# Kernel optimization log

Hardware: AMD Instinct MI355X
Metric: run time of the kernel (lower is better)

The kernel has to match this reference:

```python
import jax, jax.numpy as jnp
import numpy as np

N_NODES = 100000
N_EDGES = 1600000
D_FEAT = 64


def setup_inputs() -> dict:
    key = jax.random.key(0)
    k1, k2 = jax.random.split(key)
    x = jax.random.normal(k1, (N_NODES, D_FEAT), dtype=jnp.float32)
    edge_index = jax.random.randint(k2, (2, N_EDGES), 0, N_NODES, dtype=jnp.int64)
    return {"x": x, "edge_index": edge_index}


def reference(x, edge_index):
    # LightGCN propagation: out = D^{-1/2} A D^{-1/2} x with A given in COO form.
    row, col = edge_index[0], edge_index[1]
    n = x.shape[0]
    # deg[i] = number of edges with row == i (torch.sparse.sum over dim=1 of ones)
    deg = jax.ops.segment_sum(jnp.ones_like(row, dtype=x.dtype), row, num_segments=n)
    deg_inv_sqrt = jnp.where(deg > 0, jax.lax.rsqrt(jnp.maximum(deg, 1.0)), 0.0)
    norm = deg_inv_sqrt[row] * deg_inv_sqrt[col]  # [E]
    # SpMM: out[row] += norm * x[col]  (gather-scale-scatter-reduce)
    messages = norm[:, None] * x[col]  # [E, d]
    out = jax.ops.segment_sum(messages, row, num_segments=n)  # [N, d]
    return out
```

## Files before the change

### kernel.cpp

```cpp
#include <hip/hip_runtime.h>
#include <hip/hip_fp16.h>

#define N_NODES 100000
#define D_FEAT 64
#define RPB 256
#define NB ((N_NODES + RPB - 1) / RPB)
#define CAP 6144
#define NCH 391
#define COL_BITS 17
#define COL_MASK ((1 << COL_BITS) - 1)

typedef float vfloat4 __attribute__((ext_vector_type(4)));

__global__ void __launch_bounds__(256)
count_kernel(const int* __restrict__ row, int* __restrict__ cnt, int E) {
    __shared__ int h[NB];
    int t = threadIdx.x, c = blockIdx.x;
    for (int i = t; i < NB; i += 256) h[i] = 0;
    __syncthreads();
    int ce = (E + NCH - 1) / NCH;
    int lo = c * ce;
    int hi = min(lo + ce, E);
    for (int e = lo + t; e < hi; e += 256)
        atomicAdd(&h[row[e] >> 8], 1);
    __syncthreads();
    for (int i = t; i < NB; i += 256)
        cnt[c * NB + i] = h[i];
}

__global__ void __launch_bounds__(512)
colscan_kernel(int* __restrict__ cnt, int* __restrict__ bucketCnt) {
    __shared__ int s[512];
    int b = blockIdx.x, t = threadIdx.x;
    int v = (t < NCH) ? cnt[t * NB + b] : 0;
    s[t] = v;
    __syncthreads();
    for (int o = 1; o < 512; o <<= 1) {
        int u = (t >= o) ? s[t - o] : 0;
        __syncthreads();
        s[t] += u;
        __syncthreads();
    }
    if (t < NCH) cnt[t * NB + b] = s[t] - v;
    if (t == NCH - 1) bucketCnt[b] = s[t];
}

__global__ void __launch_bounds__(256)
part_kernel(const int* __restrict__ row, const int* __restrict__ col,
            const int* __restrict__ cnt,
            int* __restrict__ packed, int E) {
    __shared__ int h[NB];
    __shared__ int rbase[NB];
    int t = threadIdx.x, c = blockIdx.x;
    for (int i = t; i < NB; i += 256) {
        h[i] = 0;
        rbase[i] = cnt[c * NB + i];
    }
    __syncthreads();
    int ce = (E + NCH - 1) / NCH;
    int lo = c * ce;
    int hi = min(lo + ce, E);
    for (int e = lo + t; e < hi; e += 256) {
        int r = row[e], cc = col[e];
        int bk = r >> 8;
        int pos = rbase[bk] + atomicAdd(&h[bk], 1);
        if (pos < CAP)
            packed[bk * CAP + pos] = ((r & (RPB - 1)) << COL_BITS) | cc;
    }
}

__global__ void __launch_bounds__(512)
csr_build_kernel(int* __restrict__ packed,
                 const int* __restrict__ bucketCnt,
                 int4* __restrict__ rowSED,
                 const float* __restrict__ x, __half* __restrict__ xs, int N) {
    __shared__ int ebuf[CAP];
    __shared__ int sbuf[CAP];
    __shared__ int cnt[RPB];
    __shared__ int scn[RPB];
    __shared__ int cur[RPB];
    __shared__ float disS[RPB];
    int b = blockIdx.x, t = threadIdx.x;
    int base = b * CAP;
    int n = min(bucketCnt[b], CAP);
    for (int i = t; i < n; i += 512) ebuf[i] = packed[base + i];
    if (t < RPB) cnt[t] = 0;
    __syncthreads();
    for (int i = t; i < n; i += 512)
        atomicAdd(&cnt[ebuf[i] >> COL_BITS], 1);
    __syncthreads();
    int v = 0;
    if (t < RPB) { v = cnt[t]; scn[t] = v; }
    __syncthreads();
    for (int o = 1; o < RPB; o <<= 1) {
        int u = 0;
        if (t < RPB && t >= o) u = scn[t - o];
        __syncthreads();
        if (t < RPB) scn[t] += u;
        __syncthreads();
    }
    if (t < RPB) {
        int ex = scn[t] - v;
        cur[t] = ex;
        float d = (v > 0) ? rsqrtf((float)v) : 0.0f;
        disS[t] = d;
        int r = b * RPB + t;
        if (r < N)
            rowSED[r] = make_int4(base + ex, base + ex + v, __float_as_int(d), 0);
    }
    __syncthreads();
    for (int i = t; i < n; i += 512) {
        int p = ebuf[i];
        int lr = p >> COL_BITS;
        int pos = atomicAdd(&cur[lr], 1);
        sbuf[pos] = p & COL_MASK;
    }
    __syncthreads();
    for (int i = t; i < n; i += 512)
        packed[base + i] = sbuf[i];
    long long rowBase = (long long)b * RPB;
    for (int i = t; i < RPB * (D_FEAT / 4); i += 512) {
        int lr = i >> 4;
        long long rr = rowBase + lr;
        if (rr < N) {
            const vfloat4* xp = (const vfloat4*)(x + (rr << 6) + ((i & 15) << 2));
            vfloat4 vv = __builtin_nontemporal_load(xp);
            float dd = disS[lr];
            __half2 h0 = __floats2half2_rn(dd * vv.x, dd * vv.y);
            __half2 h1 = __floats2half2_rn(dd * vv.z, dd * vv.w);
            uint2 u;
            u.x = *(unsigned int*)&h0;
            u.y = *(unsigned int*)&h1;
            *(uint2*)(xs + (rr << 6) + ((i & 15) << 2)) = u;
        }
    }
}

__device__ __forceinline__ void fmap(__half2* a, uint4 v, __half2 w2) {
    __half2* hp = (__half2*)&v;
    a[0] = __hfma2(hp[0], w2, a[0]);
    a[1] = __hfma2(hp[1], w2, a[1]);
    a[2] = __hfma2(hp[2], w2, a[2]);
    a[3] = __hfma2(hp[3], w2, a[3]);
}
__device__ __forceinline__ void addp(__half2* a, uint4 v) {
    __half2* hp = (__half2*)&v;
    a[0] = __hadd2(a[0], hp[0]);
    a[1] = __hadd2(a[1], hp[1]);
    a[2] = __hadd2(a[2], hp[2]);
    a[3] = __hadd2(a[3], hp[3]);
}

__device__ __forceinline__ void row_slow(const __half* __restrict__ xs,
                                         const int* __restrict__ csr_col,
                                         int s, int e, int g, int q, __half2* acc) {
    int j = s;
    for (; j + 32 <= e; j += 32) {
        int c0 = csr_col[j + g];
        int c1 = csr_col[j + 8 + g];
        int c2 = csr_col[j + 16 + g];
        int c3 = csr_col[j + 24 + g];
        uint4 v0 = *(const uint4*)(xs + (c0 << 6) + (q << 3));
        uint4 v1 = *(const uint4*)(xs + (c1 << 6) + (q << 3));
        uint4 v2 = *(const uint4*)(xs + (c2 << 6) + (q << 3));
        uint4 v3 = *(const uint4*)(xs + (c3 << 6) + (q << 3));
        addp(acc, v0); addp(acc, v1); addp(acc, v2); addp(acc, v3);
    }
    int last = e - 1;
    int n0 = j + g, n1 = n0 + 8, n2 = n0 + 16, n3 = n0 + 24;
    int i0 = max(min(n0, last), 0);
    int i1 = max(min(n1, last), 0);
    int i2 = max(min(n2, last), 0);
    int i3 = max(min(n3, last), 0);
    int c0 = csr_col[i0] & COL_MASK;
    int c1 = csr_col[i1] & COL_MASK;
    int c2 = csr_col[i2] & COL_MASK;
    int c3 = csr_col[i3] & COL_MASK;
    uint4 v0 = *(const uint4*)(xs + (c0 << 6) + (q << 3));
    uint4 v1 = *(const uint4*)(xs + (c1 << 6) + (q << 3));
    uint4 v2 = *(const uint4*)(xs + (c2 << 6) + (q << 3));
    uint4 v3 = *(const uint4*)(xs + (c3 << 6) + (q << 3));
    __half2 w0 = __float2half2_rn((n0 < e) ? 1.0f : 0.0f);
    __half2 w1 = __float2half2_rn((n1 < e) ? 1.0f : 0.0f);
    __half2 w2 = __float2half2_rn((n2 < e) ? 1.0f : 0.0f);
    __half2 w3 = __float2half2_rn((n3 < e) ? 1.0f : 0.0f);
    fmap(acc, v0, w0); fmap(acc, v1, w1); fmap(acc, v2, w2); fmap(acc, v3, w3);
}

__global__ void __launch_bounds__(512)
spmm_h8x2_kernel(const __half* __restrict__ xs,
                 const int4* __restrict__ rowSED,
                 const int* __restrict__ csr_col,
                 float* __restrict__ out, int N) {
    int wv = (int)((blockIdx.x * (long long)blockDim.x + threadIdx.x) >> 6);
    int r0 = wv * 2;
    if (r0 >= N) return;
    int r1 = r0 + 1;
    bool has1 = (r1 < N);
    int lane = threadIdx.x & 63;
    int g = lane >> 3;
    int q = lane & 7;
    int4 sed0 = rowSED[r0];
    int4 sed1 = has1 ? rowSED[r1] : make_int4(0, 0, 0, 0);
    int s0 = sed0.x, e0 = sed0.y;
    int s1 = sed1.x, e1 = sed1.y;
    __half2 z = __float2half2_rn(0.f);
    __half2 a0[4] = {z, z, z, z};
    __half2 a1[4] = {z, z, z, z};

    if (max(e0 - s0, e1 - s1) <= 32) {
        int l0 = e0 - 1, l1 = e1 - 1;
        int m00 = s0 + g, m01 = m00 + 8, m02 = m00 + 16, m03 = m00 + 24;
        int m10 = s1 + g, m11 = m10 + 8, m12 = m10 + 16, m13 = m10 + 24;
        int i00 = max(min(m00, l0), 0), i01 = max(min(m01, l0), 0);
        int i02 = max(min(m02, l0), 0), i03 = max(min(m03, l0), 0);
        int i10 = max(min(m10, l1), 0), i11 = max(min(m11, l1), 0);
        int i12 = max(min(m12, l1), 0), i13 = max(min(m13, l1), 0);
        int c00 = csr_col[i00] & COL_MASK, c01 = csr_col[i01] & COL_MASK;
        int c02 = csr_col[i02] & COL_MASK, c03 = csr_col[i03] & COL_MASK;
        int c10 = csr_col[i10] & COL_MASK, c11 = csr_col[i11] & COL_MASK;
        int c12 = csr_col[i12] & COL_MASK, c13 = csr_col[i13] & COL_MASK;
        uint4 v00 = *(const uint4*)(xs + (c00 << 6) + (q << 3));
        uint4 v01 = *(const uint4*)(xs + (c01 << 6) + (q << 3));
        uint4 v02 = *(const uint4*)(xs + (c02 << 6) + (q << 3));
        uint4 v03 = *(const uint4*)(xs + (c03 << 6) + (q << 3));
        uint4 v10 = *(const uint4*)(xs + (c10 << 6) + (q << 3));
        uint4 v11 = *(const uint4*)(xs + (c11 << 6) + (q << 3));
        uint4 v12 = *(const uint4*)(xs + (c12 << 6) + (q << 3));
        uint4 v13 = *(const uint4*)(xs + (c13 << 6) + (q << 3));
        __half2 w00 = __float2half2_rn((m00 < e0) ? 1.0f : 0.0f);
        __half2 w01 = __float2half2_rn((m01 < e0) ? 1.0f : 0.0f);
        __half2 w02 = __float2half2_rn((m02 < e0) ? 1.0f : 0.0f);
        __half2 w03 = __float2half2_rn((m03 < e0) ? 1.0f : 0.0f);
        __half2 w10 = __float2half2_rn((m10 < e1) ? 1.0f : 0.0f);
        __half2 w11 = __float2half2_rn((m11 < e1) ? 1.0f : 0.0f);
        __half2 w12 = __float2half2_rn((m12 < e1) ? 1.0f : 0.0f);
        __half2 w13 = __float2half2_rn((m13 < e1) ? 1.0f : 0.0f);
        fmap(a0, v00, w00); fmap(a0, v01, w01); fmap(a0, v02, w02); fmap(a0, v03, w03);
        fmap(a1, v10, w10); fmap(a1, v11, w11); fmap(a1, v12, w12); fmap(a1, v13, w13);
    } else {
        row_slow(xs, csr_col, s0, e0, g, q, a0);
        if (has1) row_slow(xs, csr_col, s1, e1, g, q, a1);
    }

    #pragma unroll
    for (int k = 0; k < 4; ++k) {
        int a = *(int*)&a0[k];
        int b8 = __shfl_xor(a, 8);  a0[k] = __hadd2(a0[k], *(__half2*)&b8);
        a = *(int*)&a0[k];
        int b16 = __shfl_xor(a, 16); a0[k] = __hadd2(a0[k], *(__half2*)&b16);
        a = *(int*)&a0[k];
        int b32 = __shfl_xor(a, 32); a0[k] = __hadd2(a0[k], *(__half2*)&b32);
        a = *(int*)&a1[k];
        int d8 = __shfl_xor(a, 8);  a1[k] = __hadd2(a1[k], *(__half2*)&d8);
        a = *(int*)&a1[k];
        int d16 = __shfl_xor(a, 16); a1[k] = __hadd2(a1[k], *(__half2*)&d16);
        a = *(int*)&a1[k];
        int d32 = __shfl_xor(a, 32); a1[k] = __hadd2(a1[k], *(__half2*)&d32);
    }
    if (g == 0) {
        float dr = __int_as_float(sed0.z);
        float2 f0 = __half22float2(a0[0]);
        float2 f1 = __half22float2(a0[1]);
        float2 f2 = __half22float2(a0[2]);
        float2 f3 = __half22float2(a0[3]);
        vfloat4 o0, o1;
        o0.x = dr * f0.x; o0.y = dr * f0.y; o0.z = dr * f1.x; o0.w = dr * f1.y;
        o1.x = dr * f2.x; o1.y = dr * f2.y; o1.z = dr * f3.x; o1.w = dr * f3.y;
        float* op = out + ((long long)r0 << 6) + (q << 3);
        __builtin_nontemporal_store(o0, (vfloat4*)op);
        __builtin_nontemporal_store(o1, (vfloat4*)(op + 4));
    } else if (g == 1 && has1) {
        float dr = __int_as_float(sed1.z);
        float2 f0 = __half22float2(a1[0]);
        float2 f1 = __half22float2(a1[1]);
        float2 f2 = __half22float2(a1[2]);
        float2 f3 = __half22float2(a1[3]);
        vfloat4 o0, o1;
        o0.x = dr * f0.x; o0.y = dr * f0.y; o0.z = dr * f1.x; o0.w = dr * f1.y;
        o1.x = dr * f2.x; o1.y = dr * f2.y; o1.z = dr * f3.x; o1.w = dr * f3.y;
        float* op = out + ((long long)r1 << 6) + (q << 3);
        __builtin_nontemporal_store(o0, (vfloat4*)op);
        __builtin_nontemporal_store(o1, (vfloat4*)(op + 4));
    }
}

__global__ void fb_deg_kernel(const int* __restrict__ row, float* __restrict__ deg, int E) {
    int i = blockIdx.x * blockDim.x + threadIdx.x;
    int stride = gridDim.x * blockDim.x;
    for (; i < E; i += stride) atomicAdd(&deg[row[i]], 1.0f);
}
__global__ void fb_dis_kernel(float* __restrict__ deg, int N) {
    int i = blockIdx.x * blockDim.x + threadIdx.x;
    if (i < N) { float d = deg[i]; deg[i] = (d > 0.0f) ? rsqrtf(d) : 0.0f; }
}
__global__ void fb_scatter_kernel(const float* __restrict__ x, const int* __restrict__ row,
                                  const int* __restrict__ col, const float* __restrict__ dis,
                                  float* __restrict__ out, long long total) {
    long long i = (long long)blockIdx.x * blockDim.x + threadIdx.x;
    long long stride = (long long)gridDim.x * blockDim.x;
    for (; i < total; i += stride) {
        int e = (int)(i >> 6);
        int d = (int)(i & 63);
        int r = row[e];
        int c = col[e];
        atomicAdd(&out[(long long)r * D_FEAT + d], dis[r] * dis[c] * x[(long long)c * D_FEAT + d]);
    }
}

extern "C" void kernel_launch(void* const* d_in, const int* in_sizes, int n_in,
                              void* d_out, int out_size, void* d_ws, size_t ws_size,
                              hipStream_t stream) {
    const float* x  = (const float*)d_in[0];
    const int*   ei = (const int*)d_in[1];
    int E = in_sizes[1] / 2;
    const int* row = ei;
    const int* col = ei + E;
    float* out = (float*)d_out;
    const int N = N_NODES;

    size_t need = (size_t)NB * CAP * 4 + (size_t)N * D_FEAT * 2
                + (size_t)N * 16 + (size_t)NCH * NB * 4 + (size_t)NB * 4;

    if (ws_size >= need) {
        char* ws = (char*)d_ws;
        int*    packed    = (int*)ws;    ws += (size_t)NB * CAP * 4;
        __half* xs        = (__half*)ws; ws += (size_t)N * D_FEAT * 2;
        int4*   rowSED    = (int4*)ws;   ws += (size_t)N * 16;
        int*    cnt       = (int*)ws;    ws += (size_t)NCH * NB * 4;
        int*    bucketCnt = (int*)ws;

        count_kernel<<<NCH, 256, 0, stream>>>(row, cnt, E);
        colscan_kernel<<<NB, 512, 0, stream>>>(cnt, bucketCnt);
        part_kernel<<<NCH, 256, 0, stream>>>(row, col, cnt, packed, E);
        csr_build_kernel<<<NB, 512, 0, stream>>>(packed, bucketCnt, rowSED, x, xs, N);
        int waves = (N + 1) / 2;
        spmm_h8x2_kernel<<<(waves + 7) / 8, 512, 0, stream>>>(xs, rowSED, packed, out, N);
        return;
    }

    float* deg = (float*)d_ws;
    (void)hipMemsetAsync(out, 0, (size_t)out_size * sizeof(float), stream);
    (void)hipMemsetAsync(deg, 0, (size_t)N * sizeof(float), stream);
    fb_deg_kernel<<<2048, 256, 0, stream>>>(row, deg, E);
    fb_dis_kernel<<<(N + 255) / 256, 256, 0, stream>>>(deg, N);
    fb_scatter_kernel<<<4096, 256, 0, stream>>>(x, row, col, deg, out, (long long)E * D_FEAT);
}
```

Measured before the change: 78.53 us.

## Fuse per-bucket CSR sort into SpMM kernel using shared-memory column lists

Moves the per-bucket counting sort out of the build kernel and into the SpMM kernel, which now keeps each bucket's sorted column indices in LDS and processes its 256 rows directly. The build kernel becomes a light degree and x-scaling pass, and the rowSED array plus the write-back of sorted packed data to global memory are removed. The SpMM kernel now runs only NB (391) blocks of 512 threads with about 50KB of LDS each, which lowers occupancy and parallelism compared with one wave per two rows across the whole grid. Degree counting is also done twice.

```diff
diff --git a/kernel.cpp b/kernel.cpp
--- a/kernel.cpp
+++ b/kernel.cpp
@@ -70,54 +70,23 @@
 }
 
 __global__ void __launch_bounds__(512)
-csr_build_kernel(int* __restrict__ packed,
-                 const int* __restrict__ bucketCnt,
-                 int4* __restrict__ rowSED,
-                 const float* __restrict__ x, __half* __restrict__ xs, int N) {
-    __shared__ int ebuf[CAP];
-    __shared__ int sbuf[CAP];
+rowdis_conv_kernel(const int* __restrict__ packed, const int* __restrict__ bucketCnt,
+                   const float* __restrict__ x, __half* __restrict__ xs, int N) {
     __shared__ int cnt[RPB];
-    __shared__ int scn[RPB];
-    __shared__ int cur[RPB];
     __shared__ float disS[RPB];
     int b = blockIdx.x, t = threadIdx.x;
     int base = b * CAP;
     int n = min(bucketCnt[b], CAP);
-    for (int i = t; i < n; i += 512) ebuf[i] = packed[base + i];
     if (t < RPB) cnt[t] = 0;
     __syncthreads();
     for (int i = t; i < n; i += 512)
-        atomicAdd(&cnt[ebuf[i] >> COL_BITS], 1);
-    __syncthreads();
-    int v = 0;
-    if (t < RPB) { v = cnt[t]; scn[t] = v; }
-    __syncthreads();
-    for (int o = 1; o < RPB; o <<= 1) {
-        int u = 0;
-        if (t < RPB && t >= o) u = scn[t - o];
-        __syncthreads();
-        if (t < RPB) scn[t] += u;
-        __syncthreads();
-    }
+        atomicAdd(&cnt[packed[base + i] >> COL_BITS], 1);
+    __syncthreads();
     if (t < RPB) {
-        int ex = scn[t] - v;
-        cur[t] = ex;
-        float d = (v > 0) ? rsqrtf((float)v) : 0.0f;
-        disS[t] = d;
-        int r = b * RPB + t;
-        if (r < N)
-            rowSED[r] = make_int4(base + ex, base + ex + v, __float_as_int(d), 0);
-    }
-    __syncthreads();
-    for (int i = t; i < n; i += 512) {
-        int p = ebuf[i];
-        int lr = p >> COL_BITS;
-        int pos = atomicAdd(&cur[lr], 1);
-        sbuf[pos] = p & COL_MASK;
-    }
-    __syncthreads();
-    for (int i = t; i < n; i += 512)
-        packed[base + i] = sbuf[i];
+        int v = cnt[t];
+        disS[t] = (v > 0) ? rsqrtf((float)v) : 0.0f;
+    }
+    __syncthreads();
     long long rowBase = (long long)b * RPB;
     for (int i = t; i < RPB * (D_FEAT / 4); i += 512) {
         int lr = i >> 4;
@@ -143,145 +112,133 @@
     a[2] = __hfma2(hp[2], w2, a[2]);
     a[3] = __hfma2(hp[3], w2, a[3]);
 }
-__device__ __forceinline__ void addp(__half2* a, uint4 v) {
-    __half2* hp = (__half2*)&v;
-    a[0] = __hadd2(a[0], hp[0]);
-    a[1] = __hadd2(a[1], hp[1]);
-    a[2] = __hadd2(a[2], hp[2]);
-    a[3] = __hadd2(a[3], hp[3]);
-}
-
-__device__ __forceinline__ void row_slow(const __half* __restrict__ xs,
-                                         const int* __restrict__ csr_col,
-                                         int s, int e, int g, int q, __half2* acc) {
-    int j = s;
-    for (; j + 32 <= e; j += 32) {
-        int c0 = csr_col[j + g];
-        int c1 = csr_col[j + 8 + g];
-        int c2 = csr_col[j + 16 + g];
-        int c3 = csr_col[j + 24 + g];
-        uint4 v0 = *(const uint4*)(xs + (c0 << 6) + (q << 3));
-        uint4 v1 = *(const uint4*)(xs + (c1 << 6) + (q << 3));
-        uint4 v2 = *(const uint4*)(xs + (c2 << 6) + (q << 3));
-        uint4 v3 = *(const uint4*)(xs + (c3 << 6) + (q << 3));
-        addp(acc, v0); addp(acc, v1); addp(acc, v2); addp(acc, v3);
-    }
-    int last = e - 1;
-    int n0 = j + g, n1 = n0 + 8, n2 = n0 + 16, n3 = n0 + 24;
-    int i0 = max(min(n0, last), 0);
-    int i1 = max(min(n1, last), 0);
-    int i2 = max(min(n2, last), 0);
-    int i3 = max(min(n3, last), 0);
-    int c0 = csr_col[i0] & COL_MASK;
-    int c1 = csr_col[i1] & COL_MASK;
-    int c2 = csr_col[i2] & COL_MASK;
-    int c3 = csr_col[i3] & COL_MASK;
-    uint4 v0 = *(const uint4*)(xs + (c0 << 6) + (q << 3));
-    uint4 v1 = *(const uint4*)(xs + (c1 << 6) + (q << 3));
-    uint4 v2 = *(const uint4*)(xs + (c2 << 6) + (q << 3));
-    uint4 v3 = *(const uint4*)(xs + (c3 << 6) + (q << 3));
-    __half2 w0 = __float2half2_rn((n0 < e) ? 1.0f : 0.0f);
-    __half2 w1 = __float2half2_rn((n1 < e) ? 1.0f : 0.0f);
-    __half2 w2 = __float2half2_rn((n2 < e) ? 1.0f : 0.0f);
-    __half2 w3 = __float2half2_rn((n3 < e) ? 1.0f : 0.0f);
-    fmap(acc, v0, w0); fmap(acc, v1, w1); fmap(acc, v2, w2); fmap(acc, v3, w3);
-}
 
 __global__ void __launch_bounds__(512)
-spmm_h8x2_kernel(const __half* __restrict__ xs,
-                 const int4* __restrict__ rowSED,
-                 const int* __restrict__ csr_col,
-                 float* __restrict__ out, int N) {
-    int wv = (int)((blockIdx.x * (long long)blockDim.x + threadIdx.x) >> 6);
-    int r0 = wv * 2;
-    if (r0 >= N) return;
-    int r1 = r0 + 1;
-    bool has1 = (r1 < N);
-    int lane = threadIdx.x & 63;
+csr_spmm_kernel(int* __restrict__ packed,
+                const int* __restrict__ bucketCnt,
+                const __half* __restrict__ xs,
+                float* __restrict__ out, int N) {
+    __shared__ int ebuf[CAP];
+    __shared__ int sbuf[CAP];
+    __shared__ int rs[RPB];
+    __shared__ int rv[RPB];
+    __shared__ int cur[RPB];
+    __shared__ int scn[RPB];
+    __shared__ float disS[RPB];
+    int b = blockIdx.x, t = threadIdx.x;
+    int base = b * CAP;
+    int n = min(bucketCnt[b], CAP);
+    for (int i = t; i < n; i += 512) ebuf[i] = packed[base + i];
+    if (t < RPB) { rs[t] = 0; rv[t] = 0; cur[t] = 0; scn[t] = 0; }
+    __syncthreads();
+    for (int i = t; i < n; i += 512)
+        atomicAdd(&rv[ebuf[i] >> COL_BITS], 1);
+    __syncthreads();
+    int v = 0;
+    if (t < RPB) { v = rv[t]; scn[t] = v; }
+    __syncthreads();
+    for (int o = 1; o < RPB; o <<= 1) {
+        int u = 0;
+        if (t < RPB && t >= o) u = scn[t - o];
+        __syncthreads();
+        if (t < RPB) scn[t] += u;
+        __syncthreads();
+    }
+    if (t < RPB) {
+        int ex = scn[t] - v;
+        rs[t] = ex;
+        cur[t] = ex;
+        disS[t] = (v > 0) ? rsqrtf((float)v) : 0.0f;
+    }
+    __syncthreads();
+    for (int i = t; i < n; i += 512) {
+        int p = ebuf[i];
+        int lr = p >> COL_BITS;
+        int pos = atomicAdd(&cur[lr], 1);
+        sbuf[pos] = p & COL_MASK;
+    }
+    __syncthreads();
+
+    int wv = t >> 6;
+    int lane = t & 63;
     int g = lane >> 3;
     int q = lane & 7;
-    int4 sed0 = rowSED[r0];
-    int4 sed1 = has1 ? rowSED[r1] : make_int4(0, 0, 0, 0);
-    int s0 = sed0.x, e0 = sed0.y;
-    int s1 = sed1.x, e1 = sed1.y;
+    long long rowBase = (long long)b * RPB;
     __half2 z = __float2half2_rn(0.f);
-    __half2 a0[4] = {z, z, z, z};
-    __half2 a1[4] = {z, z, z, z};
-
-    if (max(e0 - s0, e1 - s1) <= 32) {
-        int l0 = e0 - 1, l1 = e1 - 1;
-        int m00 = s0 + g, m01 = m00 + 8, m02 = m00 + 16, m03 = m00 + 24;
-        int m10 = s1 + g, m11 = m10 + 8, m12 = m10 + 16, m13 = m10 + 24;
-        int i00 = max(min(m00, l0), 0), i01 = max(min(m01, l0), 0);
-        int i02 = max(min(m02, l0), 0), i03 = max(min(m03, l0), 0);
-        int i10 = max(min(m10, l1), 0), i11 = max(min(m11, l1), 0);
-        int i12 = max(min(m12, l1), 0), i13 = max(min(m13, l1), 0);
-        int c00 = csr_col[i00] & COL_MASK, c01 = csr_col[i01] & COL_MASK;
-        int c02 = csr_col[i02] & COL_MASK, c03 = csr_col[i03] & COL_MASK;
-        int c10 = csr_col[i10] & COL_MASK, c11 = csr_col[i11] & COL_MASK;
-        int c12 = csr_col[i12] & COL_MASK, c13 = csr_col[i13] & COL_MASK;
-        uint4 v00 = *(const uint4*)(xs + (c00 << 6) + (q << 3));
-        uint4 v01 = *(const uint4*)(xs + (c01 << 6) + (q << 3));
-        uint4 v02 = *(const uint4*)(xs + (c02 << 6) + (q << 3));
-        uint4 v03 = *(const uint4*)(xs + (c03 << 6) + (q << 3));
-        uint4 v10 = *(const uint4*)(xs + (c10 << 6) + (q << 3));
-        uint4 v11 = *(const uint4*)(xs + (c11 << 6) + (q << 3));
-        uint4 v12 = *(const uint4*)(xs + (c12 << 6) + (q << 3));
-        uint4 v13 = *(const uint4*)(xs + (c13 << 6) + (q << 3));
-        __half2 w00 = __float2half2_rn((m00 < e0) ? 1.0f : 0.0f);
-        __half2 w01 = __float2half2_rn((m01 < e0) ? 1.0f : 0.0f);
-        __half2 w02 = __float2half2_rn((m02 < e0) ? 1.0f : 0.0f);
-        __half2 w03 = __float2half2_rn((m03 < e0) ? 1.0f : 0.0f);
-        __half2 w10 = __float2half2_rn((m10 < e1) ? 1.0f : 0.0f);
-        __half2 w11 = __float2half2_rn((m11 < e1) ? 1.0f : 0.0f);
-        __half2 w12 = __float2half2_rn((m12 < e1) ? 1.0f : 0.0f);
-        __half2 w13 = __float2half2_rn((m13 < e1) ? 1.0f : 0.0f);
-        fmap(a0, v00, w00); fmap(a0, v01, w01); fmap(a0, v02, w02); fmap(a0, v03, w03);
-        fmap(a1, v10, w10); fmap(a1, v11, w11); fmap(a1, v12, w12); fmap(a1, v13, w13);
-    } else {
-        row_slow(xs, csr_col, s0, e0, g, q, a0);
-        if (has1) row_slow(xs, csr_col, s1, e1, g, q, a1);
-    }
-
-    #pragma unroll
-    for (int k = 0; k < 4; ++k) {
-        int a = *(int*)&a0[k];
-        int b8 = __shfl_xor(a, 8);  a0[k] = __hadd2(a0[k], *(__half2*)&b8);
-        a = *(int*)&a0[k];
-        int b16 = __shfl_xor(a, 16); a0[k] = __hadd2(a0[k], *(__half2*)&b16);
-        a = *(int*)&a0[k];
-        int b32 = __shfl_xor(a, 32); a0[k] = __hadd2(a0[k], *(__half2*)&b32);
-        a = *(int*)&a1[k];
-        int d8 = __shfl_xor(a, 8);  a1[k] = __hadd2(a1[k], *(__half2*)&d8);
-        a = *(int*)&a1[k];
-        int d16 = __shfl_xor(a, 16); a1[k] = __hadd2(a1[k], *(__half2*)&d16);
-        a = *(int*)&a1[k];
-        int d32 = __shfl_xor(a, 32); a1[k] = __hadd2(a1[k], *(__half2*)&d32);
-    }
-    if (g == 0) {
-        float dr = __int_as_float(sed0.z);
-        float2 f0 = __half22float2(a0[0]);
-        float2 f1 = __half22float2(a0[1]);
-        float2 f2 = __half22float2(a0[2]);
-        float2 f3 = __half22float2(a0[3]);
-        vfloat4 o0, o1;
-        o0.x = dr * f0.x; o0.y = dr * f0.y; o0.z = dr * f1.x; o0.w = dr * f1.y;
-        o1.x = dr * f2.x; o1.y = dr * f2.y; o1.z = dr * f3.x; o1.w = dr * f3.y;
-        float* op = out + ((long long)r0 << 6) + (q << 3);
-        __builtin_nontemporal_store(o0, (vfloat4*)op);
-        __builtin_nontemporal_store(o1, (vfloat4*)(op + 4));
-    } else if (g == 1 && has1) {
-        float dr = __int_as_float(sed1.z);
-        float2 f0 = __half22float2(a1[0]);
-        float2 f1 = __half22float2(a1[1]);
-        float2 f2 = __half22float2(a1[2]);
-        float2 f3 = __half22float2(a1[3]);
-        vfloat4 o0, o1;
-        o0.x = dr * f0.x; o0.y = dr * f0.y; o0.z = dr * f1.x; o0.w = dr * f1.y;
-        o1.x = dr * f2.x; o1.y = dr * f2.y; o1.z = dr * f3.x; o1.w = dr * f3.y;
-        float* op = out + ((long long)r1 << 6) + (q << 3);
-        __builtin_nontemporal_store(o0, (vfloat4*)op);
-        __builtin_nontemporal_store(o1, (vfloat4*)(op + 4));
+    #pragma unroll 1
+    for (int p = 0; p < 16; ++p) {
+        int lr0 = wv * 32 + 2 * p;
+        int lr1 = lr0 + 1;
+        int s0 = rs[lr0], v0 = rv[lr0];
+        int s1 = rs[lr1], v1 = rv[lr1];
+        __half2 a0[4] = {z, z, z, z};
+        __half2 a1[4] = {z, z, z, z};
+        int mx = max(v0, v1);
+        for (int j = 0; j < mx; j += 32) {
+            int c0[4], c1[4];
+            __half2 w0[4], w1[4];
+            #pragma unroll
+            for (int k = 0; k < 4; ++k) {
+                int n0 = j + g + 8 * k;
+                int i0 = s0 + max(min(n0, v0 - 1), 0);
+                c0[k] = sbuf[min(i0, CAP - 1)];
+                w0[k] = __float2half2_rn((n0 < v0) ? 1.0f : 0.0f);
+                int i1 = s1 + max(min(n0, v1 - 1), 0);
+                c1[k] = sbuf[min(i1, CAP - 1)];
+                w1[k] = __float2half2_rn((n0 < v1) ? 1.0f : 0.0f);
+            }
+            uint4 g0[4], g1[4];
+            #pragma unroll
+            for (int k = 0; k < 4; ++k)
+                g0[k] = *(const uint4*)(xs + (c0[k] << 6) + (q << 3));
+            #pragma unroll
+            for (int k = 0; k < 4; ++k)
+                g1[k] = *(const uint4*)(xs + (c1[k] << 6) + (q << 3));
+            #pragma unroll
+            for (int k = 0; k < 4; ++k) { fmap(a0, g0[k], w0[k]); fmap(a1, g1[k], w1[k]); }
+        }
+        #pragma unroll
+        for (int k = 0; k < 4; ++k) {
+            int a = *(int*)&a0[k];
+            int b8 = __shfl_xor(a, 8);   a0[k] = __hadd2(a0[k], *(__half2*)&b8);
+            a = *(int*)&a0[k];
+            int b16 = __shfl_xor(a, 16); a0[k] = __hadd2(a0[k], *(__half2*)&b16);
+            a = *(int*)&a0[k];
+            int b32 = __shfl_xor(a, 32); a0[k] = __hadd2(a0[k], *(__half2*)&b32);
+            a = *(int*)&a1[k];
+            int d8 = __shfl_xor(a, 8);   a1[k] = __hadd2(a1[k], *(__half2*)&d8);
+            a = *(int*)&a1[k];
+            int d16 = __shfl_xor(a, 16); a1[k] = __hadd2(a1[k], *(__half2*)&d16);
+            a = *(int*)&a1[k];
+            int d32 = __shfl_xor(a, 32); a1[k] = __hadd2(a1[k], *(__half2*)&d32);
+        }
+        long long r0 = rowBase + lr0;
+        long long r1 = rowBase + lr1;
+        if (g == 0 && r0 < N) {
+            float dr = disS[lr0];
+            float2 f0 = __half22float2(a0[0]);
+            float2 f1 = __half22float2(a0[1]);
+            float2 f2 = __half22float2(a0[2]);
+            float2 f3 = __half22float2(a0[3]);
+            vfloat4 o0, o1;
+            o0.x = dr * f0.x; o0.y = dr * f0.y; o0.z = dr * f1.x; o0.w = dr * f1.y;
+            o1.x = dr * f2.x; o1.y = dr * f2.y; o1.z = dr * f3.x; o1.w = dr * f3.y;
+            float* op = out + (r0 << 6) + (q << 3);
+            __builtin_nontemporal_store(o0, (vfloat4*)op);
+            __builtin_nontemporal_store(o1, (vfloat4*)(op + 4));
+        } else if (g == 1 && r1 < N) {
+            float dr = disS[lr1];
+            float2 f0 = __half22float2(a1[0]);
+            float2 f1 = __half22float2(a1[1]);
+            float2 f2 = __half22float2(a1[2]);
+            float2 f3 = __half22float2(a1[3]);
+            vfloat4 o0, o1;
+            o0.x = dr * f0.x; o0.y = dr * f0.y; o0.z = dr * f1.x; o0.w = dr * f1.y;
+            o1.x = dr * f2.x; o1.y = dr * f2.y; o1.z = dr * f3.x; o1.w = dr * f3.y;
+            float* op = out + (r1 << 6) + (q << 3);
+            __builtin_nontemporal_store(o0, (vfloat4*)op);
+            __builtin_nontemporal_store(o1, (vfloat4*)(op + 4));
+        }
     }
 }
 
@@ -320,22 +277,20 @@
     const int N = N_NODES;
 
     size_t need = (size_t)NB * CAP * 4 + (size_t)N * D_FEAT * 2
-                + (size_t)N * 16 + (size_t)NCH * NB * 4 + (size_t)NB * 4;
+                + (size_t)NCH * NB * 4 + (size_t)NB * 4;
 
     if (ws_size >= need) {
         char* ws = (char*)d_ws;
         int*    packed    = (int*)ws;    ws += (size_t)NB * CAP * 4;
         __half* xs        = (__half*)ws; ws += (size_t)N * D_FEAT * 2;
-        int4*   rowSED    = (int4*)ws;   ws += (size_t)N * 16;
         int*    cnt       = (int*)ws;    ws += (size_t)NCH * NB * 4;
         int*    bucketCnt = (int*)ws;
 
         count_kernel<<<NCH, 256, 0, stream>>>(row, cnt, E);
         colscan_kernel<<<NB, 512, 0, stream>>>(cnt, bucketCnt);
         part_kernel<<<NCH, 256, 0, stream>>>(row, col, cnt, packed, E);
-        csr_build_kernel<<<NB, 512, 0, stream>>>(packed, bucketCnt, rowSED, x, xs, N);
-        int waves = (N + 1) / 2;
-        spmm_h8x2_kernel<<<(waves + 7) / 8, 512, 0, stream>>>(xs, rowSED, packed, out, N);
+        rowdis_conv_kernel<<<NB, 512, 0, stream>>>(packed, bucketCnt, x, xs, N);
+        csr_spmm_kernel<<<NB, 512, 0, stream>>>(packed, bucketCnt, xs, out, N);
         return;
     }
 
```

Result: slower. 82.39 us (+4.9%).

## Replace count+scan bucketing with per-chunk global atomic cursor reservation

Applied to the files above, without the earlier changes.

Removes the separate count and column-scan kernels. Each partition block now builds a local histogram of its edge chunk and reserves space in each bucket with one global atomicAdd per non-empty bucket, then scatters. This saves a full pass over row plus a scan kernel and a launch, at the cost of global atomics and a nondeterministic edge order within buckets. The order change can alter floating-point summation order.

```diff
diff --git a/kernel.cpp b/kernel.cpp
--- a/kernel.cpp
+++ b/kernel.cpp
@@ -6,72 +6,49 @@
 #define RPB 256
 #define NB ((N_NODES + RPB - 1) / RPB)
 #define CAP 6144
-#define NCH 391
+#define CHUNK 4096
 #define COL_BITS 17
 #define COL_MASK ((1 << COL_BITS) - 1)
 
 typedef float vfloat4 __attribute__((ext_vector_type(4)));
 
-__global__ void __launch_bounds__(256)
-count_kernel(const int* __restrict__ row, int* __restrict__ cnt, int E) {
-    __shared__ int h[NB];
-    int t = threadIdx.x, c = blockIdx.x;
-    for (int i = t; i < NB; i += 256) h[i] = 0;
-    __syncthreads();
-    int ce = (E + NCH - 1) / NCH;
-    int lo = c * ce;
-    int hi = min(lo + ce, E);
-    for (int e = lo + t; e < hi; e += 256)
-        atomicAdd(&h[row[e] >> 8], 1);
-    __syncthreads();
-    for (int i = t; i < NB; i += 256)
-        cnt[c * NB + i] = h[i];
-}
-
-__global__ void __launch_bounds__(512)
-colscan_kernel(int* __restrict__ cnt, int* __restrict__ bucketCnt) {
-    __shared__ int s[512];
-    int b = blockIdx.x, t = threadIdx.x;
-    int v = (t < NCH) ? cnt[t * NB + b] : 0;
-    s[t] = v;
-    __syncthreads();
-    for (int o = 1; o < 512; o <<= 1) {
-        int u = (t >= o) ? s[t - o] : 0;
-        __syncthreads();
-        s[t] += u;
-        __syncthreads();
-    }
-    if (t < NCH) cnt[t * NB + b] = s[t] - v;
-    if (t == NCH - 1) bucketCnt[b] = s[t];
+__global__ void zero_kernel(int* __restrict__ p, int n) {
+    int i = blockIdx.x * blockDim.x + threadIdx.x;
+    if (i < n) p[i] = 0;
 }
 
 __global__ void __launch_bounds__(256)
 part_kernel(const int* __restrict__ row, const int* __restrict__ col,
-            const int* __restrict__ cnt,
+            int* __restrict__ bucketCursor,
             int* __restrict__ packed, int E) {
     __shared__ int h[NB];
     __shared__ int rbase[NB];
-    int t = threadIdx.x, c = blockIdx.x;
+    int t = threadIdx.x;
+    for (int i = t; i < NB; i += 256) h[i] = 0;
+    __syncthreads();
+    int lo = blockIdx.x * CHUNK;
+    int hi = min(lo + CHUNK, E);
+    for (int e = lo + t; e < hi; e += 256)
+        atomicAdd(&h[row[e] >> 8], 1);
+    __syncthreads();
     for (int i = t; i < NB; i += 256) {
+        int c2 = h[i];
+        rbase[i] = c2 ? atomicAdd(&bucketCursor[i], c2) : 0;
         h[i] = 0;
-        rbase[i] = cnt[c * NB + i];
-    }
-    __syncthreads();
-    int ce = (E + NCH - 1) / NCH;
-    int lo = c * ce;
-    int hi = min(lo + ce, E);
+    }
+    __syncthreads();
     for (int e = lo + t; e < hi; e += 256) {
-        int r = row[e], cc = col[e];
+        int r = row[e], c = col[e];
         int bk = r >> 8;
         int pos = rbase[bk] + atomicAdd(&h[bk], 1);
         if (pos < CAP)
-            packed[bk * CAP + pos] = ((r & (RPB - 1)) << COL_BITS) | cc;
+            packed[bk * CAP + pos] = ((r & (RPB - 1)) << COL_BITS) | c;
     }
 }
 
 __global__ void __launch_bounds__(512)
 csr_build_kernel(int* __restrict__ packed,
-                 const int* __restrict__ bucketCnt,
+                 const int* __restrict__ bucketCursor,
                  int4* __restrict__ rowSED,
                  const float* __restrict__ x, __half* __restrict__ xs, int N) {
     __shared__ int ebuf[CAP];
@@ -82,7 +59,7 @@
     __shared__ float disS[RPB];
     int b = blockIdx.x, t = threadIdx.x;
     int base = b * CAP;
-    int n = min(bucketCnt[b], CAP);
+    int n = min(bucketCursor[b], CAP);
     for (int i = t; i < n; i += 512) ebuf[i] = packed[base + i];
     if (t < RPB) cnt[t] = 0;
     __syncthreads();
@@ -320,20 +297,19 @@
     const int N = N_NODES;
 
     size_t need = (size_t)NB * CAP * 4 + (size_t)N * D_FEAT * 2
-                + (size_t)N * 16 + (size_t)NCH * NB * 4 + (size_t)NB * 4;
+                + (size_t)N * 16 + (size_t)NB * 4;
 
     if (ws_size >= need) {
         char* ws = (char*)d_ws;
-        int*    packed    = (int*)ws;    ws += (size_t)NB * CAP * 4;
-        __half* xs        = (__half*)ws; ws += (size_t)N * D_FEAT * 2;
-        int4*   rowSED    = (int4*)ws;   ws += (size_t)N * 16;
-        int*    cnt       = (int*)ws;    ws += (size_t)NCH * NB * 4;
-        int*    bucketCnt = (int*)ws;
-
-        count_kernel<<<NCH, 256, 0, stream>>>(row, cnt, E);
-        colscan_kernel<<<NB, 512, 0, stream>>>(cnt, bucketCnt);
-        part_kernel<<<NCH, 256, 0, stream>>>(row, col, cnt, packed, E);
-        csr_build_kernel<<<NB, 512, 0, stream>>>(packed, bucketCnt, rowSED, x, xs, N);
+        int*    packed       = (int*)ws;    ws += (size_t)NB * CAP * 4;
+        __half* xs           = (__half*)ws; ws += (size_t)N * D_FEAT * 2;
+        int4*   rowSED       = (int4*)ws;   ws += (size_t)N * 16;
+        int*    bucketCursor = (int*)ws;
+
+        zero_kernel<<<1, 512, 0, stream>>>(bucketCursor, NB);
+        int nChunks = (E + CHUNK - 1) / CHUNK;
+        part_kernel<<<nChunks, 256, 0, stream>>>(row, col, bucketCursor, packed, E);
+        csr_build_kernel<<<NB, 512, 0, stream>>>(packed, bucketCursor, rowSED, x, xs, N);
         int waves = (N + 1) / 2;
         spmm_h8x2_kernel<<<(waves + 7) / 8, 512, 0, stream>>>(xs, rowSED, packed, out, N);
         return;
```

Result: slower. 80.14 us (+2.1%).
